# Optimization experiments

Measured on AMD Instinct MI355X. Metric: run time of the kernel, lower is better.

## Reference

```python
import jax, jax.numpy as jnp
import numpy as np

EMBED_DIM = 256
NUM_HEADS = 8
NUM_LEVELS = 4
NUM_POINTS = 4
OFFSET_SCALE = 0.5
SUM_PTS = NUM_LEVELS * NUM_POINTS  # 16
TOTAL_PTS = NUM_HEADS * SUM_PTS    # 128
SPATIAL = ((80, 80), (40, 40), (20, 20), (10, 10))
LEN_V = sum(h * w for h, w in SPATIAL)  # 8500


def _offset_bias():
    # replicates _reset_parameters grid init for sampling_offsets.bias
    thetas = jnp.arange(NUM_HEADS, dtype=jnp.float32) * (2.0 * np.pi / NUM_HEADS)
    grid = jnp.stack([jnp.cos(thetas), jnp.sin(thetas)], -1)              # [H,2]
    grid = grid / jnp.abs(grid).max(-1, keepdims=True)
    grid = jnp.tile(grid[:, None, :], (1, SUM_PTS, 1))                    # [H,SUM_PTS,2]
    scaling = jnp.concatenate([jnp.arange(1, NUM_POINTS + 1, dtype=jnp.float32)
                               for _ in range(NUM_LEVELS)]).reshape(1, -1, 1)
    return (grid * scaling).reshape(-1)                                   # [TOTAL_PTS*2]


def setup_inputs() -> dict:
    key = jax.random.key(0)
    ks = jax.random.split(key, 8)
    bs, Lq, D = 16, 300, EMBED_DIM
    query = jax.random.normal(ks[0], (bs, Lq, D), dtype=jnp.float32)
    # (cx, cy, w, h) in (0,1); keep w,h modest so samples mostly land in-bounds
    rp = jax.random.uniform(ks[1], (bs, Lq, 1, 4), dtype=jnp.float32)
    reference_points = jnp.concatenate([rp[..., :2], 0.1 + 0.4 * rp[..., 2:]], axis=-1)
    value = jax.random.normal(ks[2], (bs, LEN_V, D), dtype=jnp.float32)
    # params (torch Linear convention: W is [out, in]); small random instead of exact
    # zero-init so the math is non-degenerate, bias uses the faithful grid init
    W_off = 0.01 * jax.random.normal(ks[3], (TOTAL_PTS * 2, D), dtype=jnp.float32)
    b_off = _offset_bias()
    W_attn = 0.01 * jax.random.normal(ks[4], (TOTAL_PTS, D), dtype=jnp.float32)
    b_attn = jnp.zeros((TOTAL_PTS,), dtype=jnp.float32)
    xav = float(np.sqrt(6.0 / (D + D)))
    W_val = jax.random.uniform(ks[5], (D, D), minval=-xav, maxval=xav, dtype=jnp.float32)
    b_val = jnp.zeros((D,), dtype=jnp.float32)
    W_out = jax.random.uniform(ks[6], (D, D), minval=-xav, maxval=xav, dtype=jnp.float32)
    b_out = jnp.zeros((D,), dtype=jnp.float32)
    return {"query": query, "reference_points": reference_points, "value": value,
            "W_off": W_off, "b_off": b_off, "W_attn": W_attn, "b_attn": b_attn,
            "W_val": W_val, "b_val": b_val, "W_out": W_out, "b_out": b_out,
            "value_spatial_shapes": SPATIAL}


def bilinear_sample(img, grid):
    # img: [N, C, H, W]; grid: [N, Q, P, 2] in [-1,1] -> [N, C, Q, P]
    # matches F.grid_sample(mode='bilinear', padding_mode='zeros', align_corners=False)
    N, C, H, W = img.shape
    x = (grid[..., 0] + 1.0) * (W * 0.5) - 0.5
    y = (grid[..., 1] + 1.0) * (H * 0.5) - 0.5
    x0 = jnp.floor(x)
    y0 = jnp.floor(y)
    wx = (x - x0)[:, None]  # [N,1,Q,P]
    wy = (y - y0)[:, None]
    flat = img.reshape(N, C, H * W)

    def gather(xi, yi):
        valid = (xi >= 0) & (xi <= W - 1) & (yi >= 0) & (yi <= H - 1)
        idx = (jnp.clip(yi, 0, H - 1) * W + jnp.clip(xi, 0, W - 1)).astype(jnp.int32)
        v = jnp.take_along_axis(flat, idx.reshape(N, 1, -1), axis=2)
        return v.reshape(N, C, *idx.shape[1:]) * valid.astype(img.dtype)[:, None]

    v00 = gather(x0, y0)
    v01 = gather(x0 + 1, y0)
    v10 = gather(x0, y0 + 1)
    v11 = gather(x0 + 1, y0 + 1)
    return (v00 * (1 - wx) * (1 - wy) + v01 * wx * (1 - wy)
            + v10 * (1 - wx) * wy + v11 * wx * wy)


def reference(query, reference_points, value, W_off, b_off, W_attn, b_attn,
              W_val, b_val, W_out, b_out, value_spatial_shapes):
    bs, Lq, D = query.shape
    H, hd = NUM_HEADS, D // NUM_HEADS
    Lv = value.shape[1]
    v = (value @ W_val.T + b_val).reshape(bs, Lv, H, hd)
    off = (query @ W_off.T + b_off).reshape(bs, Lq, H, SUM_PTS, 2)
    aw = jax.nn.softmax((query @ W_attn.T + b_attn).reshape(bs, Lq, H, SUM_PTS), axis=-1)
    # reference_points: [bs, Lq, 1, 4] (cx, cy, w, h); num_points_scale = 1/P per point
    nps = jnp.full((SUM_PTS, 1), 1.0 / NUM_POINTS, dtype=query.dtype)
    offset = off * nps * reference_points[:, :, None, :, 2:] * OFFSET_SCALE
    loc = reference_points[:, :, None, :, :2] + offset      # [bs,Lq,H,SUM_PTS,2]
    grids = (2.0 * loc - 1.0).transpose(0, 2, 1, 3, 4).reshape(bs * H, Lq, SUM_PTS, 2)
    v_flat = v.transpose(0, 2, 3, 1).reshape(bs * H, hd, Lv)
    outs = []
    sv = sp = 0
    for (h, w) in value_spatial_shapes:
        value_l = v_flat[:, :, sv:sv + h * w].reshape(bs * H, hd, h, w)
        grid_l = grids[:, :, sp:sp + NUM_POINTS, :]
        outs.append(bilinear_sample(value_l, grid_l))        # [bs*H, hd, Lq, P]
        sv += h * w
        sp += NUM_POINTS
    sampled = jnp.concatenate(outs, axis=-1)                 # [bs*H, hd, Lq, SUM_PTS]
    aw_ = aw.transpose(0, 2, 1, 3).reshape(bs * H, 1, Lq, SUM_PTS)
    out = (sampled * aw_).sum(-1).reshape(bs, H * hd, Lq).transpose(0, 2, 1)
    return out @ W_out.T + b_out
```

## Files before the change

kernel.cpp:

```cpp
#include <hip/hip_runtime.h>
#include <hip/hip_bf16.h>

#define BS 16
#define LQ 300
#define DIM 256
#define NH 8
#define HD 32
#define SUMP 16
#define LV 8500
#define NQ (BS*LQ)
#define MROWS (BS*LV)
#define RS 40
#define RS2 260
#define CS 264

typedef __bf16 bf16x4 __attribute__((ext_vector_type(4)));
typedef __bf16 bf16x8 __attribute__((ext_vector_type(8)));
typedef float f32x4 __attribute__((ext_vector_type(4)));

__device__ __forceinline__ bf16x4 cvt8B(float4 a) {
    bf16x4 r;
    r[0] = (__bf16)a.x; r[1] = (__bf16)a.y; r[2] = (__bf16)a.z; r[3] = (__bf16)a.w;
    return r;
}
__device__ __forceinline__ bf16x8 cvt16B(float4 a, float4 b) {
    bf16x8 r;
    r[0] = (__bf16)a.x; r[1] = (__bf16)a.y; r[2] = (__bf16)a.z; r[3] = (__bf16)a.w;
    r[4] = (__bf16)b.x; r[5] = (__bf16)b.y; r[6] = (__bf16)b.z; r[7] = (__bf16)b.w;
    return r;
}

__global__ __launch_bounds__(256) void k_cvtB(
    const float* __restrict__ Wv, bf16x8* __restrict__ out)
{
    const int idx = blockIdx.x * 256 + threadIdx.x;
    const int n = idx & 255, kp = idx >> 8;
    const float4 a0 = *(const float4*)(Wv + n * 256 + kp * 8);
    const float4 a1 = *(const float4*)(Wv + n * 256 + kp * 8 + 4);
    out[kp * 256 + n] = cvt16B(a0, a1);
}

__device__ __forceinline__ void small_gemm_body(
    unsigned short* SH, const float* A_, const float* W_, int M_, int bm,
    int t, f32x4 (&acc)[4][4])
{
    unsigned short* const A0 = SH;
    unsigned short* const A1 = SH + 5120;
    unsigned short* const B0 = SH + 10240;
    unsigned short* const B1 = SH + 15360;
    const int lane = t & 63, wid = t >> 6;
    const int wm = (wid >> 1) * 64, wn = (wid & 1) * 64;
    const int fra = lane & 15;
    const int koff = (lane >> 4) * 8;
    const int srow = t >> 3;
    const int scol = (t & 7) * 4;
    unsigned aoff[4];
    const float* pb0 = W_ + (long)srow * 256 + scol;
    #pragma unroll
    for (int u = 0; u < 4; ++u) {
        long gr = (long)bm * 128 + u * 32 + srow;
        if (gr > M_ - 1) gr = M_ - 1;
        aoff[u] = (unsigned)(gr * 256 + scol);
    }
    const int lw = srow * RS + scol;
    {
        #pragma unroll
        for (int u = 0; u < 4; ++u) {
            float4 a = *(const float4*)(A_ + aoff[u]);
            float4 b = *(const float4*)(pb0 + u * 32 * 256);
            *(bf16x4*)&A0[lw + u * 32 * RS] = cvt8B(a);
            *(bf16x4*)&B0[lw + u * 32 * RS] = cvt8B(b);
        }
    }
    __syncthreads();
    #pragma unroll
    for (int kt = 0; kt < 8; ++kt) {
        unsigned short* Ac = (kt & 1) ? A1 : A0;
        unsigned short* An = (kt & 1) ? A0 : A1;
        unsigned short* Bc = (kt & 1) ? B1 : B0;
        unsigned short* Bn = (kt & 1) ? B0 : B1;
        float4 na[4], nb[4];
        if (kt < 7) {
            const int k0 = (kt + 1) * 32;
            #pragma unroll
            for (int u = 0; u < 4; ++u) {
                na[u] = *(const float4*)(A_ + aoff[u] + k0);
                nb[u] = *(const float4*)(pb0 + u * 32 * 256 + k0);
            }
        }
        bf16x8 af[4], bfv[4];
        #pragma unroll
        for (int i = 0; i < 4; ++i)
            af[i] = *(const bf16x8*)&Ac[(wm + i * 16 + fra) * RS + koff];
        #pragma unroll
        for (int j = 0; j < 4; ++j)
            bfv[j] = *(const bf16x8*)&Bc[(wn + j * 16 + fra) * RS + koff];
        #pragma unroll
        for (int i = 0; i < 4; ++i)
            #pragma unroll
            for (int j = 0; j < 4; ++j)
                acc[i][j] = __builtin_amdgcn_mfma_f32_16x16x32_bf16(
                    bfv[j], af[i], acc[i][j], 0, 0, 0);
        if (kt < 7) {
            #pragma unroll
            for (int u = 0; u < 4; ++u) {
                *(bf16x4*)&An[lw + u * 32 * RS] = cvt8B(na[u]);
                *(bf16x4*)&Bn[lw + u * 32 * RS] = cvt8B(nb[u]);
            }
        }
        __syncthreads();
    }
}

__device__ __forceinline__ void valgemm_body(
    unsigned short* SH, int bm, int t,
    const float* value, const bf16x8* wvbp, const float* bv,
    unsigned short* vout)
{
    const int lane = t & 63, wid = t >> 6;
    const int wn = wid * 64;
    const int fra = lane & 15;
    const int g = lane >> 4;

    const float* src = value + (long)bm * 32 * 256;
    float4 s0[8];
    #pragma unroll
    for (int u = 0; u < 8; ++u) s0[u] = *(const float4*)(src + (u * 256 + t) * 4);
    #pragma unroll
    for (int u = 0; u < 8; ++u) {
        const int f = u * 256 + t, row = f >> 6, col4 = f & 63;
        *(bf16x4*)&SH[row * RS2 + col4 * 4] = cvt8B(s0[u]);
    }
    __syncthreads();

    f32x4 acc[2][4] = {};
    const bf16x8* wvb_base = wvbp + wn + fra + g * 256;
    const int koff = g * 8;
    #pragma unroll
    for (int kt = 0; kt < 8; ++kt) {
        bf16x8 bfv[4];
        #pragma unroll
        for (int j = 0; j < 4; ++j) bfv[j] = wvb_base[kt * 1024 + j * 16];
        bf16x8 af[2];
        #pragma unroll
        for (int i = 0; i < 2; ++i)
            af[i] = *(const bf16x8*)&SH[(i * 16 + fra) * RS2 + kt * 32 + koff];
        #pragma unroll
        for (int i = 0; i < 2; ++i)
            #pragma unroll
            for (int j = 0; j < 4; ++j)
                acc[i][j] = __builtin_amdgcn_mfma_f32_16x16x32_bf16(
                    bfv[j], af[i], acc[i][j], 0, 0, 0);
    }

    __syncthreads();
    const int nreg = g * 4;
    #pragma unroll
    for (int j = 0; j < 4; ++j) {
        const int n0 = wn + j * 16 + nreg;
        const float4 bj = *(const float4*)&bv[n0];
        #pragma unroll
        for (int i = 0; i < 2; ++i) {
            const int m = i * 16 + fra;
            float4 v;
            v.x = acc[i][j][0] + bj.x;
            v.y = acc[i][j][1] + bj.y;
            v.z = acc[i][j][2] + bj.z;
            v.w = acc[i][j][3] + bj.w;
            *(bf16x4*)&SH[m * CS + n0] = cvt8B(v);
        }
    }
    __syncthreads();
    #pragma unroll
    for (int u = 0; u < 4; ++u) {
        const int f = u * 256 + t;
        const int row = f >> 5, c16 = f & 31;
        *(uint4*)&vout[((long)bm * 32 + row) * 256 + c16 * 8] =
            *(const uint4*)&SH[row * CS + c16 * 8];
    }
}

__global__ __launch_bounds__(256, 4) void k_fused1(
    const float* __restrict__ value, const bf16x8* __restrict__ wvbp,
    const float* __restrict__ bv, unsigned short* __restrict__ vout,
    const float* __restrict__ query,
    const float* __restrict__ Woff, const float* __restrict__ boff,
    const float* __restrict__ Wattn, const float* __restrict__ battn,
    const float* __restrict__ refp,
    float* __restrict__ loc, float* __restrict__ aw)
{
    __shared__ unsigned short SH[20480];
    const int t = threadIdx.x;
    const int id = blockIdx.x;

    if (id >= 114) {
        valgemm_body(SH, id - 114, t, value, wvbp, bv, vout);
        return;
    }

    const int bm = id / 3, bn = id % 3;
    const float* Wsel = (bn < 2) ? (Woff + (long)bn * 128 * 256) : Wattn;
    f32x4 acc[4][4] = {};
    small_gemm_body(SH, query, Wsel, NQ, bm, t, acc);

    const int lane = t & 63, wid = t >> 6;
    const int wm = (wid >> 1) * 64, wn = (wid & 1) * 64;
    const int fra = lane & 15;
    const int nreg = (lane >> 4) * 4;
    if (bn < 2) {
        float4 bj[4];
        #pragma unroll
        for (int j = 0; j < 4; ++j)
            bj[j] = *(const float4*)&boff[bn * 128 + wn + j * 16 + nreg];
        #pragma unroll
        for (int i = 0; i < 4; ++i) {
            const long grow = (long)bm * 128 + wm + i * 16 + fra;
            if (grow < NQ) {
                const float4 rp = *(const float4*)&refp[grow * 4];
                const float sx = 0.125f * rp.z, sy = 0.125f * rp.w;
                #pragma unroll
                for (int j = 0; j < 4; ++j) {
                    float4 v;
                    v.x = rp.x + (acc[i][j][0] + bj[j].x) * sx;
                    v.y = rp.y + (acc[i][j][1] + bj[j].y) * sy;
                    v.z = rp.x + (acc[i][j][2] + bj[j].z) * sx;
                    v.w = rp.y + (acc[i][j][3] + bj[j].w) * sy;
                    *(float4*)&loc[grow * 256 + bn * 128 + wn + j * 16 + nreg] = v;
                }
            }
        }
    } else {
        #pragma unroll
        for (int i = 0; i < 4; ++i) {
            const long grow = (long)bm * 128 + wm + i * 16 + fra;
            #pragma unroll
            for (int j = 0; j < 4; ++j) {
                const int n0 = wn + j * 16 + nreg;
                const float4 bj = *(const float4*)&battn[n0];
                float vx = acc[i][j][0] + bj.x;
                float vy = acc[i][j][1] + bj.y;
                float vz = acc[i][j][2] + bj.z;
                float vw = acc[i][j][3] + bj.w;
                float mx = fmaxf(fmaxf(vx, vy), fmaxf(vz, vw));
                mx = fmaxf(mx, __shfl_xor(mx, 16));
                mx = fmaxf(mx, __shfl_xor(mx, 32));
                float ex = expf(vx - mx), ey = expf(vy - mx);
                float ez = expf(vz - mx), ew = expf(vw - mx);
                float s = ex + ey + ez + ew;
                s += __shfl_xor(s, 16);
                s += __shfl_xor(s, 32);
                const float inv = 1.f / s;
                if (grow < NQ) {
                    const int hh = (wn >> 4) + j;
                    float4 o;
                    o.x = ex * inv; o.y = ey * inv; o.z = ez * inv; o.w = ew * inv;
                    *(float4*)&aw[(grow * 8 + hh) * 16 + nreg] = o;
                }
            }
        }
    }
}

__global__ __launch_bounds__(256) void k_gemm_out(
    const float* __restrict__ A, const float* __restrict__ W,
    const float* __restrict__ bias, float* __restrict__ out)
{
    __shared__ unsigned short SH[20480];
    const int t = threadIdx.x;
    const int bm = blockIdx.x, bn = blockIdx.y;
    const float* Wsel = W + (long)bn * 128 * 256;
    f32x4 acc[4][4] = {};
    small_gemm_body(SH, A, Wsel, NQ, bm, t, acc);

    const int lane = t & 63, wid = t >> 6;
    const int wm = (wid >> 1) * 64, wn = (wid & 1) * 64;
    const int fra = lane & 15;
    const int nreg = (lane >> 4) * 4;
    #pragma unroll
    for (int j = 0; j < 4; ++j) {
        const int nn = bn * 128 + wn + j * 16 + nreg;
        const float4 bj = *(const float4*)&bias[nn];
        #pragma unroll
        for (int i = 0; i < 4; ++i) {
            const long grow = (long)bm * 128 + wm + i * 16 + fra;
            if (grow < NQ) {
                float4 v;
                v.x = acc[i][j][0] + bj.x;
                v.y = acc[i][j][1] + bj.y;
                v.z = acc[i][j][2] + bj.z;
                v.w = acc[i][j][3] + bj.w;
                *(float4*)&out[grow * 256 + nn] = v;
            }
        }
    }
}

__global__ __launch_bounds__(256) void k_sample(
    const unsigned short* __restrict__ vbf, const float* __restrict__ loc,
    const float* __restrict__ aw, float* __restrict__ sampled)
{
    const int t = threadIdx.x;
    const int wid = t >> 6, lane = t & 63;
    const int id = blockIdx.x * 4 + wid;
    const int h = id & 7;
    const int qg = id >> 3;
    const int b = qg / LQ;
    const int cp = lane & 15;
    const int q = lane >> 4;

    const int WLs[4] = {80, 40, 20, 10};
    const int SVs[4] = {0, 6400, 8000, 8400};
    const int Wl = WLs[q];
    const unsigned short* vb = vbf + (long)b * LV * 256 + (long)SVs[q] * 256 + h * 32 + cp * 2;

    const float* locp = loc + (long)id * 32 + q * 8;
    const float* awp  = aw  + (long)id * 16 + q * 4;

    const float4 l01 = *(const float4*)locp;
    const float4 l23 = *(const float4*)(locp + 4);
    const float4 aw4 = *(const float4*)awp;
    const float lx[4] = {l01.x, l01.z, l23.x, l23.z};
    const float ly[4] = {l01.y, l01.w, l23.y, l23.w};
    const float awv[4] = {aw4.x, aw4.y, aw4.z, aw4.w};

    float ax = 0.f, ay = 0.f;
    unsigned uu[4][4];
    float wc[4][4];
    #pragma unroll
    for (int k = 0; k < 4; ++k) {
        const float x = lx[k] * Wl - 0.5f, y = ly[k] * Wl - 0.5f;
        const float x0f = floorf(x), y0f = floorf(y);
        const float wx = x - x0f, wy = y - y0f;
        const int x0 = (int)x0f, y0 = (int)y0f;
        const int x1 = x0 + 1, y1 = y0 + 1;
        const int xc0 = min(max(x0, 0), Wl - 1), xc1 = min(max(x1, 0), Wl - 1);
        const int yc0 = min(max(y0, 0), Wl - 1), yc1 = min(max(y1, 0), Wl - 1);
        const float fx0 = (x0 >= 0 && x0 < Wl) ? 1.f : 0.f;
        const float fx1 = (x1 >= 0 && x1 < Wl) ? 1.f : 0.f;
        const float fy0 = (y0 >= 0 && y0 < Wl) ? 1.f : 0.f;
        const float fy1 = (y1 >= 0 && y1 < Wl) ? 1.f : 0.f;
        wc[k][0] = awv[k] * (1.f - wy) * (1.f - wx) * fy0 * fx0;
        wc[k][1] = awv[k] * (1.f - wy) * wx * fy0 * fx1;
        wc[k][2] = awv[k] * wy * (1.f - wx) * fy1 * fx0;
        wc[k][3] = awv[k] * wy * wx * fy1 * fx1;
        uu[k][0] = *(const unsigned*)&vb[(unsigned)((yc0 * Wl + xc0) * 256)];
        uu[k][1] = *(const unsigned*)&vb[(unsigned)((yc0 * Wl + xc1) * 256)];
        uu[k][2] = *(const unsigned*)&vb[(unsigned)((yc1 * Wl + xc0) * 256)];
        uu[k][3] = *(const unsigned*)&vb[(unsigned)((yc1 * Wl + xc1) * 256)];
    }
    #pragma unroll
    for (int k = 0; k < 4; ++k)
        #pragma unroll
        for (int c = 0; c < 4; ++c) {
            ax = fmaf(wc[k][c], __uint_as_float((uu[k][c] & 0xffffu) << 16), ax);
            ay = fmaf(wc[k][c], __uint_as_float(uu[k][c] & 0xffff0000u), ay);
        }
    ax += __shfl_xor(ax, 16); ay += __shfl_xor(ay, 16);
    ax += __shfl_xor(ax, 32); ay += __shfl_xor(ay, 32);
    if (q == 0) {
        float2 o; o.x = ax; o.y = ay;
        *(float2*)&sampled[(long)qg * 256 + h * 32 + cp * 2] = o;
    }
}

extern "C" void kernel_launch(void* const* d_in, const int* in_sizes, int n_in,
                              void* d_out, int out_size, void* d_ws, size_t ws_size,
                              hipStream_t stream)
{
    const float* query = (const float*)d_in[0];
    const float* refp  = (const float*)d_in[1];
    const float* value = (const float*)d_in[2];
    const float* Woff  = (const float*)d_in[3];
    const float* boff  = (const float*)d_in[4];
    const float* Wattn = (const float*)d_in[5];
    const float* battn = (const float*)d_in[6];
    const float* Wval  = (const float*)d_in[7];
    const float* bval  = (const float*)d_in[8];
    const float* Wout  = (const float*)d_in[9];
    const float* bout  = (const float*)d_in[10];

    char* ws = (char*)d_ws;
    unsigned short* vbf = (unsigned short*)ws;
    float* loc     = (float*)(ws + 69632000);
    float* aw      = (float*)(ws + 74547200);
    bf16x8* wvb    = (bf16x8*)(ws + 77004800);
    float* sampled = (float*)(ws + 77004800);

    hipLaunchKernelGGL(k_cvtB, dim3(32), dim3(256), 0, stream, Wval, wvb);
    hipLaunchKernelGGL(k_fused1, dim3(4364), dim3(256), 0, stream,
                       value, wvb, bval, vbf,
                       query, Woff, boff, Wattn, battn, refp, loc, aw);
    hipLaunchKernelGGL(k_sample, dim3(9600), dim3(256), 0, stream,
                       vbf, loc, aw, sampled);
    hipLaunchKernelGGL(k_gemm_out, dim3(38, 2), dim3(256), 0, stream,
                       sampled, Wout, bout, (float*)d_out);
}
```

Measured before the change: 90.91 us.

## Make value-projection GEMM persistent with double-buffered prefetch of value tiles

Replaces the one-tile-per-block value projection (4250 blocks) with 768 persistent blocks that loop over tiles. Each block prefetches the next 32-row fp32 value tile into registers and writes it to a second LDS buffer while the current tile's MFMAs run. The goal is to hide global load latency and cut block launch overhead. LDS per block grows to about 50KB, so launch bounds drop to 3 blocks per CU, and prefetching adds register pressure.

```diff
diff --git a/kernel.cpp b/kernel.cpp
--- a/kernel.cpp
+++ b/kernel.cpp
@@ -11,8 +11,10 @@
 #define NQ (BS*LQ)
 #define MROWS (BS*LV)
 #define RS 40
-#define RS2 260
+#define AS 264
 #define CS 264
+#define NVAL 768
+#define NTILE 4250
 
 typedef __bf16 bf16x4 __attribute__((ext_vector_type(4)));
 typedef __bf16 bf16x8 __attribute__((ext_vector_type(8)));
@@ -112,75 +114,104 @@
     }
 }
 
-__device__ __forceinline__ void valgemm_body(
-    unsigned short* SH, int bm, int t,
+__device__ __forceinline__ void valgemm_persistent(
+    unsigned short* SH, int blk, int t,
     const float* value, const bf16x8* wvbp, const float* bv,
     unsigned short* vout)
 {
+    unsigned short* const Abuf[2] = { SH, SH + 32 * AS };
+    unsigned short* const Cst = SH + 64 * AS;
+
     const int lane = t & 63, wid = t >> 6;
     const int wn = wid * 64;
     const int fra = lane & 15;
     const int g = lane >> 4;
-
-    const float* src = value + (long)bm * 32 * 256;
-    float4 s0[8];
-    #pragma unroll
-    for (int u = 0; u < 8; ++u) s0[u] = *(const float4*)(src + (u * 256 + t) * 4);
-    #pragma unroll
-    for (int u = 0; u < 8; ++u) {
-        const int f = u * 256 + t, row = f >> 6, col4 = f & 63;
-        *(bf16x4*)&SH[row * RS2 + col4 * 4] = cvt8B(s0[u]);
+    const int koff = g * 8;
+
+    {
+        const float* src = value + (long)blk * 32 * 256;
+        float4 s0[8];
+        #pragma unroll
+        for (int u = 0; u < 8; ++u) s0[u] = *(const float4*)(src + (u * 256 + t) * 4);
+        #pragma unroll
+        for (int u = 0; u < 8; ++u) {
+            const int f = u * 256 + t, row = f >> 6, col4 = f & 63;
+            *(bf16x4*)&Abuf[0][row * AS + col4 * 4] = cvt8B(s0[u]);
+        }
     }
     __syncthreads();
 
-    f32x4 acc[2][4] = {};
     const bf16x8* wvb_base = wvbp + wn + fra + g * 256;
-    const int koff = g * 8;
-    #pragma unroll
-    for (int kt = 0; kt < 8; ++kt) {
-        bf16x8 bfv[4];
-        #pragma unroll
-        for (int j = 0; j < 4; ++j) bfv[j] = wvb_base[kt * 1024 + j * 16];
-        bf16x8 af[2];
-        #pragma unroll
-        for (int i = 0; i < 2; ++i)
-            af[i] = *(const bf16x8*)&SH[(i * 16 + fra) * RS2 + kt * 32 + koff];
-        #pragma unroll
-        for (int i = 0; i < 2; ++i)
-            #pragma unroll
-            for (int j = 0; j < 4; ++j)
-                acc[i][j] = __builtin_amdgcn_mfma_f32_16x16x32_bf16(
-                    bfv[j], af[i], acc[i][j], 0, 0, 0);
-    }
-
-    __syncthreads();
-    const int nreg = g * 4;
-    #pragma unroll
-    for (int j = 0; j < 4; ++j) {
-        const int n0 = wn + j * 16 + nreg;
-        const float4 bj = *(const float4*)&bv[n0];
-        #pragma unroll
-        for (int i = 0; i < 2; ++i) {
-            const int m = i * 16 + fra;
-            float4 v;
-            v.x = acc[i][j][0] + bj.x;
-            v.y = acc[i][j][1] + bj.y;
-            v.z = acc[i][j][2] + bj.z;
-            v.w = acc[i][j][3] + bj.w;
-            *(bf16x4*)&SH[m * CS + n0] = cvt8B(v);
-        }
-    }
-    __syncthreads();
-    #pragma unroll
-    for (int u = 0; u < 4; ++u) {
-        const int f = u * 256 + t;
-        const int row = f >> 5, c16 = f & 31;
-        *(uint4*)&vout[((long)bm * 32 + row) * 256 + c16 * 8] =
-            *(const uint4*)&SH[row * CS + c16 * 8];
-    }
-}
-
-__global__ __launch_bounds__(256, 4) void k_fused1(
+    int parity = 0;
+
+    for (int tile = blk; tile < NTILE; tile += NVAL) {
+        const int nxt = tile + NVAL;
+        const bool has = nxt < NTILE;
+        float4 nx[8];
+        if (has) {
+            const float* src = value + (long)nxt * 32 * 256;
+            #pragma unroll
+            for (int u = 0; u < 8; ++u) nx[u] = *(const float4*)(src + (u * 256 + t) * 4);
+        }
+
+        f32x4 acc[2][4] = {};
+        const unsigned short* Ac = Abuf[parity];
+        #pragma unroll
+        for (int kt = 0; kt < 8; ++kt) {
+            bf16x8 bfv[4];
+            #pragma unroll
+            for (int j = 0; j < 4; ++j) bfv[j] = wvb_base[kt * 1024 + j * 16];
+            bf16x8 af[2];
+            #pragma unroll
+            for (int i = 0; i < 2; ++i)
+                af[i] = *(const bf16x8*)&Ac[(i * 16 + fra) * AS + kt * 32 + koff];
+            #pragma unroll
+            for (int i = 0; i < 2; ++i)
+                #pragma unroll
+                for (int j = 0; j < 4; ++j)
+                    acc[i][j] = __builtin_amdgcn_mfma_f32_16x16x32_bf16(
+                        bfv[j], af[i], acc[i][j], 0, 0, 0);
+        }
+
+        if (has) {
+            #pragma unroll
+            for (int u = 0; u < 8; ++u) {
+                const int f = u * 256 + t, row = f >> 6, col4 = f & 63;
+                *(bf16x4*)&Abuf[parity ^ 1][row * AS + col4 * 4] = cvt8B(nx[u]);
+            }
+        }
+
+        const int nreg = g * 4;
+        #pragma unroll
+        for (int j = 0; j < 4; ++j) {
+            const int n0 = wn + j * 16 + nreg;
+            const float4 bj = *(const float4*)&bv[n0];
+            #pragma unroll
+            for (int i = 0; i < 2; ++i) {
+                const int m = i * 16 + fra;
+                float4 v;
+                v.x = acc[i][j][0] + bj.x;
+                v.y = acc[i][j][1] + bj.y;
+                v.z = acc[i][j][2] + bj.z;
+                v.w = acc[i][j][3] + bj.w;
+                *(bf16x4*)&Cst[m * CS + n0] = cvt8B(v);
+            }
+        }
+        __syncthreads();
+
+        #pragma unroll
+        for (int u = 0; u < 4; ++u) {
+            const int f = u * 256 + t;
+            const int row = f >> 5, c16 = f & 31;
+            *(uint4*)&vout[((long)tile * 32 + row) * 256 + c16 * 8] =
+                *(const uint4*)&Cst[row * CS + c16 * 8];
+        }
+        __syncthreads();
+        parity ^= 1;
+    }
+}
+
+__global__ __launch_bounds__(256, 3) void k_fused1(
     const float* __restrict__ value, const bf16x8* __restrict__ wvbp,
     const float* __restrict__ bv, unsigned short* __restrict__ vout,
     const float* __restrict__ query,
@@ -189,12 +220,12 @@
     const float* __restrict__ refp,
     float* __restrict__ loc, float* __restrict__ aw)
 {
-    __shared__ unsigned short SH[20480];
+    __shared__ unsigned short SH[96 * AS];
     const int t = threadIdx.x;
     const int id = blockIdx.x;
 
     if (id >= 114) {
-        valgemm_body(SH, id - 114, t, value, wvbp, bv, vout);
+        valgemm_persistent(SH, id - 114, t, value, wvbp, bv, vout);
         return;
     }
 
@@ -387,7 +418,7 @@
     float* sampled = (float*)(ws + 77004800);
 
     hipLaunchKernelGGL(k_cvtB, dim3(32), dim3(256), 0, stream, Wval, wvb);
-    hipLaunchKernelGGL(k_fused1, dim3(4364), dim3(256), 0, stream,
+    hipLaunchKernelGGL(k_fused1, dim3(114 + NVAL), dim3(256), 0, stream,
                        value, wvb, bval, vbf,
                        query, Woff, boff, Wattn, battn, refp, loc, aw);
     hipLaunchKernelGGL(k_sample, dim3(9600), dim3(256), 0, stream,
```

Result: slower. 179.9 us (+97.8%).
